# Kernel tuning notes

Hardware: AMD Instinct MI355X
Metric: run time of the kernel (lower is better)

Reference implementation:

```python
import jax, jax.numpy as jnp
import numpy as np
from jax import lax

# Dims from LSTMTagger class constants
B, S, LP = 1024, 128, 14       # sentences, words/sentence, padded chars/word
K, CE, WE, Lf = 3, 6, 10, 4    # char window, char emb, word emb, cnn filters
H, V, A, T = 6, 50000, 100, 135  # lstm hidden, vocab, alphabet, tagset
D = WE + Lf                     # lstm input dim = 14
LW = LP - K + 1                 # conv windows per word = 12


def setup_inputs() -> dict:
    key = jax.random.key(0)
    ks = jax.random.split(key, 14)
    n = lambda k, shp: jax.random.normal(k, shp, dtype=jnp.float32) * 0.1
    inp = {
        "word_idx": jax.random.randint(ks[0], (B, S), 0, V, dtype=jnp.int32),
        "char_idx": jax.random.randint(ks[1], (B, S, LP), 0, A, dtype=jnp.int32),
        "word_emb": n(ks[2], (V, WE)),
        "char_emb": n(ks[3], (A, CE)),
        "Wc": n(ks[4], (Lf, K * CE)),   # Conv1d(1, l, K*CE) weight, squeezed
        "bc": n(ks[5], (Lf,)),
        "Wih_f": n(ks[6], (4 * H, D)),
        "Whh_f": n(ks[7], (4 * H, H)),
        "b_f": n(ks[8], (4 * H,)),      # b_ih + b_hh fused (equivalent)
        "Wih_b": n(ks[9], (4 * H, D)),
        "Whh_b": n(ks[10], (4 * H, H)),
        "b_b": n(ks[11], (4 * H,)),
        "Wt": n(ks[12], (T, 2 * H)),
        "bt": n(ks[13], (T,)),
    }
    return inp


def _lstm_scan(xs, Wih, Whh, b):
    # xs: [S, B, D] -> hs: [S, B, H]; torch gate order i, f, g, o
    h0 = jnp.zeros((xs.shape[1], H), xs.dtype)

    def step(carry, xt):
        h, c = carry
        g = xt @ Wih.T + h @ Whh.T + b
        i, f, gg, o = jnp.split(g, 4, axis=-1)
        c = jax.nn.sigmoid(f) * c + jax.nn.sigmoid(i) * jnp.tanh(gg)
        h = jax.nn.sigmoid(o) * jnp.tanh(c)
        return (h, c), h

    _, hs = lax.scan(step, (h0, h0), xs)
    return hs


def reference(word_emb, char_emb, Wc, bc, Wih_f, Whh_f, b_f,
              Wih_b, Whh_b, b_b, Wt, bt, word_idx, char_idx):
    # per-word char CNN: sliding K-char windows, flatten, linear, max-pool
    ce = char_emb[char_idx]                              # [B,S,LP,CE]
    windows = jnp.concatenate([ce[:, :, i:i + LW] for i in range(K)], axis=-1)  # [B,S,LW,K*CE]
    phi = jnp.einsum('bswk,lk->bswl', windows, Wc) + bc  # [B,S,LW,Lf]
    char_repr = phi.max(axis=2)                          # [B,S,Lf]

    we = word_emb[word_idx]                              # [B,S,WE]
    x = jnp.concatenate([we, char_repr], axis=-1)        # [B,S,D]

    xs = x.transpose(1, 0, 2)                            # [S,B,D]
    hf = _lstm_scan(xs, Wih_f, Whh_f, b_f)               # forward direction
    hb = _lstm_scan(xs[::-1], Wih_b, Whh_b, b_b)[::-1]   # backward direction
    out = jnp.concatenate([hf, hb], axis=-1).transpose(1, 0, 2)  # [B,S,2H]

    tag_space = out @ Wt.T + bt                          # [B,S,T]
    return jax.nn.log_softmax(tag_space, axis=-1)
```

## Files before the change

### kernel.cpp

```cpp
#include <hip/hip_runtime.h>

#define B_   1024
#define S_   128
#define LP_  14
#define K_   3
#define CE_  6
#define WE_  10
#define LF_  4
#define H_   6
#define D_   14
#define T_   135
#define LW_  12
#define V_   50000
#define A_   100

static __device__ __forceinline__ float fsigm(float x) {
    return __frcp_rn(1.0f + __expf(-x));
}
static __device__ __forceinline__ float ftanh(float x) {
    return fmaf(2.0f, __frcp_rn(1.0f + __expf(-2.0f * x)), -1.0f);
}

__global__ __launch_bounds__(256) void k_el(
    const int* __restrict__ word_idx, const int* __restrict__ char_idx,
    const float* __restrict__ word_emb, const float* __restrict__ char_emb,
    const float* __restrict__ Wc, const float* __restrict__ bc,
    const float* __restrict__ Wih_f, const float* __restrict__ Whh_f, const float* __restrict__ b_f,
    const float* __restrict__ Wih_b, const float* __restrict__ Whh_b, const float* __restrict__ b_b,
    float* __restrict__ hbuf)
{
    __shared__ float s_g[4][S_][49];
    __shared__ float s_h[4][S_][12];
    __shared__ float s_ce[A_ * CE_];
    __shared__ float s_wc[LF_ * K_ * CE_];
    __shared__ float s_bc[LF_];

    int t = threadIdx.x;
    for (int e = t; e < A_ * CE_; e += 256) s_ce[e] = char_emb[e];
    if (t < LF_ * K_ * CE_) s_wc[t] = Wc[t];
    if (t < LF_) s_bc[t] = bc[t];
    __syncthreads();

    int Wbase = blockIdx.x * 512;
    #pragma unroll
    for (int rep = 0; rep < 2; ++rep) {
        int wl = t + rep * 256;
        int sent = wl >> 7;
        int step = wl & (S_ - 1);
        int w  = Wbase + wl;

        const int2* ci2 = (const int2*)(char_idx + (size_t)w * LP_);
        int idxs[LP_];
        #pragma unroll
        for (int p = 0; p < 7; ++p) {
            int2 v = ci2[p];
            idxs[2 * p] = v.x; idxs[2 * p + 1] = v.y;
        }
        float ce[LP_][CE_];
        #pragma unroll
        for (int p = 0; p < LP_; ++p) {
            int idx = idxs[p];
            idx = idx < 0 ? 0 : (idx >= A_ ? A_ - 1 : idx);
            #pragma unroll
            for (int c = 0; c < CE_; ++c) ce[p][c] = s_ce[idx * CE_ + c];
        }
        float x[D_];
        #pragma unroll
        for (int l = 0; l < LF_; ++l) {
            float acc[LW_];
            float bl = s_bc[l];
            #pragma unroll
            for (int q = 0; q < LW_; ++q) acc[q] = bl;
            #pragma unroll
            for (int kk = 0; kk < K_; ++kk) {
                #pragma unroll
                for (int c = 0; c < CE_; ++c) {
                    float wv_ = s_wc[l * (K_ * CE_) + kk * CE_ + c];
                    #pragma unroll
                    for (int q = 0; q < LW_; ++q) acc[q] = fmaf(ce[q + kk][c], wv_, acc[q]);
                }
            }
            float m = acc[0];
            #pragma unroll
            for (int q = 1; q < LW_; ++q) m = fmaxf(m, acc[q]);
            x[WE_ + l] = m;
        }
        int wi = word_idx[w];
        wi = wi < 0 ? 0 : (wi >= V_ ? V_ - 1 : wi);
        const float2* wep = (const float2*)(word_emb + (size_t)wi * WE_);
        #pragma unroll
        for (int c = 0; c < WE_ / 2; ++c) {
            float2 v = wep[c];
            x[2 * c] = v.x; x[2 * c + 1] = v.y;
        }

        #pragma unroll
        for (int r = 0; r < 4 * H_; ++r) {
            float a = b_f[r];
            #pragma unroll
            for (int k = 0; k < D_; ++k) a = fmaf(Wih_f[r * D_ + k], x[k], a);
            s_g[sent][step][r] = a;
        }
        #pragma unroll
        for (int r = 0; r < 4 * H_; ++r) {
            float a = b_b[r];
            #pragma unroll
            for (int k = 0; k < D_; ++k) a = fmaf(Wih_b[r * D_ + k], x[k], a);
            s_g[sent][step][24 + r] = a;
        }
    }
    __syncthreads();

    {
        int wv2  = t >> 6;
        int lane = t & 63;
        int dir  = lane >> 5;
        int l    = lane & 31;
        bool act = (l < H_);
        int u    = act ? l : (H_ - 1);

        const float* Whh = dir ? Whh_b : Whh_f;
        float whh[4][H_];
        #pragma unroll
        for (int j = 0; j < 4; ++j)
            #pragma unroll
            for (int k = 0; k < H_; ++k)
                whh[j][k] = Whh[(j * H_ + u) * H_ + k];

        const float* gp = &s_g[wv2][dir ? (S_ - 1) : 0][dir * 24 + u];
        int gstride = dir ? -49 : 49;

        float hv[H_];
        #pragma unroll
        for (int k = 0; k < H_; ++k) hv[k] = 0.f;
        float c = 0.f;

        float g0 = gp[0], g1 = gp[6], g2 = gp[12], g3 = gp[18];
        for (int s = 0; s < S_; ++s) {
            float ai = g0, af = g1, ag = g2, ao = g3;
            if (s + 1 < S_) {
                gp += gstride;
                g0 = gp[0]; g1 = gp[6]; g2 = gp[12]; g3 = gp[18];
            }
            #pragma unroll
            for (int k = 0; k < H_; ++k) {
                ai = fmaf(whh[0][k], hv[k], ai);
                af = fmaf(whh[1][k], hv[k], af);
                ag = fmaf(whh[2][k], hv[k], ag);
                ao = fmaf(whh[3][k], hv[k], ao);
            }
            float si = fsigm(ai);
            float sf = fsigm(af);
            float so = fsigm(ao);
            float tg = ftanh(ag);
            c = fmaf(sf, c, si * tg);
            float hu = so * ftanh(c);

            int se = dir ? (S_ - 1 - s) : s;
            if (act) s_h[wv2][se][dir * H_ + u] = hu;

            #pragma unroll
            for (int k = 0; k < H_; ++k) {
                int vf = __builtin_amdgcn_readlane(__float_as_int(hu), k);
                int vb = __builtin_amdgcn_readlane(__float_as_int(hu), 32 + k);
                hv[k] = __int_as_float(dir ? vb : vf);
            }
        }
    }
    __syncthreads();

    {
        float4* dst = (float4*)(hbuf + (size_t)blockIdx.x * 4 * S_ * 12);
        const float4* src = (const float4*)&s_h[0][0][0];
        #pragma unroll
        for (int i = 0; i < 6; ++i) dst[t + 256 * i] = src[t + 256 * i];
    }
}

__global__ __launch_bounds__(256) void k_p(
    const float* __restrict__ hbuf,
    const float* __restrict__ Wt, const float* __restrict__ bt,
    float* __restrict__ out)
{
    __shared__ float s_hb[64 * 12];
    int t = threadIdx.x;
    int ib = blockIdx.x * 64;
    {
        const float4* src = (const float4*)(hbuf + (size_t)ib * 12);
        float4* dst = (float4*)s_hb;
        if (t < 192) dst[t] = src[t];
    }
    __syncthreads();

    int lane = t & 63, wv = t >> 6;
    bool has2 = (lane < T_ - 128);
    int t2c = has2 ? (lane + 128) : (T_ - 1);

    float wA[12], wB[12], wC[12];
    #pragma unroll
    for (int jj = 0; jj < 12; ++jj) {
        wA[jj] = Wt[lane * 12 + jj];
        wB[jj] = Wt[(lane + 64) * 12 + jj];
        wC[jj] = Wt[t2c * 12 + jj];
    }
    float bA = bt[lane], bB = bt[lane + 64], bC = bt[t2c];

    int it0 = wv * 16;
    #pragma unroll 4
    for (int k = 0; k < 16; ++k) {
        int it = it0 + k;
        const float4* h4 = (const float4*)(s_hb + it * 12);
        float4 a0 = h4[0], a1 = h4[1], a2 = h4[2];
        float hv[12] = {a0.x, a0.y, a0.z, a0.w, a1.x, a1.y, a1.z, a1.w, a2.x, a2.y, a2.z, a2.w};
        float y0 = bA, y1 = bB, y2 = bC;
        #pragma unroll
        for (int jj = 0; jj < 12; ++jj) {
            y0 = fmaf(hv[jj], wA[jj], y0);
            y1 = fmaf(hv[jj], wB[jj], y1);
            y2 = fmaf(hv[jj], wC[jj], y2);
        }
        float ss = __expf(y0) + __expf(y1) + (has2 ? __expf(y2) : 0.0f);
        #pragma unroll
        for (int mk = 1; mk < 64; mk <<= 1) ss += __shfl_xor(ss, mk, 64);
        float ls = __logf(ss);
        float* op = out + (size_t)(ib + it) * T_;
        op[lane]      = y0 - ls;
        op[lane + 64] = y1 - ls;
        if (has2) op[lane + 128] = y2 - ls;
    }
}

extern "C" void kernel_launch(void* const* d_in, const int* in_sizes, int n_in,
                              void* d_out, int out_size, void* d_ws, size_t ws_size,
                              hipStream_t stream)
{
    const int* word_idx = (const int*)d_in[0];
    const int* char_idx = (const int*)d_in[1];
    const float* word_emb = (const float*)d_in[2];
    const float* char_emb = (const float*)d_in[3];
    const float* Wc    = (const float*)d_in[4];
    const float* bc    = (const float*)d_in[5];
    const float* Wih_f = (const float*)d_in[6];
    const float* Whh_f = (const float*)d_in[7];
    const float* b_f   = (const float*)d_in[8];
    const float* Wih_b = (const float*)d_in[9];
    const float* Whh_b = (const float*)d_in[10];
    const float* b_b   = (const float*)d_in[11];
    const float* Wt    = (const float*)d_in[12];
    const float* bt    = (const float*)d_in[13];

    float* hbuf = (float*)d_ws;

    k_el<<<B_ / 4, 256, 0, stream>>>(word_idx, char_idx, word_emb, char_emb, Wc, bc,
                                     Wih_f, Whh_f, b_f, Wih_b, Whh_b, b_b, hbuf);
    k_p<<<(B_ * S_) / 64, 256, 0, stream>>>(hbuf, Wt, bt, (float*)d_out);
}
```

Measured before the change: 186.9 us.

## Split fused embed+LSTM kernel into separate embed and recurrence kernels

Splits the fused embedding/CNN/input-projection plus recurrence kernel into two kernels. The first computes input gate pre-activations for all words and writes them to a global buffer laid out time-major. The second runs the recurrences with 8 sequences (both directions) per 64-thread wave, broadcasting h through shuffles and software-prefetching two steps ahead. This aims to raise occupancy and the number of concurrent recurrences, since the old kernel left most lanes idle and used large shared memory. In exchange it adds a global round trip for the gate buffer and reuses d_out as scratch when the workspace is too small.

```diff
diff --git a/kernel.cpp b/kernel.cpp
--- a/kernel.cpp
+++ b/kernel.cpp
@@ -13,6 +13,7 @@
 #define LW_  12
 #define V_   50000
 #define A_   100
+#define NSEQ (B_ * 2)
 
 static __device__ __forceinline__ float fsigm(float x) {
     return __frcp_rn(1.0f + __expf(-x));
@@ -21,160 +22,170 @@
     return fmaf(2.0f, __frcp_rn(1.0f + __expf(-2.0f * x)), -1.0f);
 }
 
-__global__ __launch_bounds__(256) void k_el(
+__global__ __launch_bounds__(256) void k_e(
     const int* __restrict__ word_idx, const int* __restrict__ char_idx,
     const float* __restrict__ word_emb, const float* __restrict__ char_emb,
     const float* __restrict__ Wc, const float* __restrict__ bc,
-    const float* __restrict__ Wih_f, const float* __restrict__ Whh_f, const float* __restrict__ b_f,
-    const float* __restrict__ Wih_b, const float* __restrict__ Whh_b, const float* __restrict__ b_b,
-    float* __restrict__ hbuf)
-{
-    __shared__ float s_g[4][S_][49];
-    __shared__ float s_h[4][S_][12];
+    const float* __restrict__ Wih_f, const float* __restrict__ b_f,
+    const float* __restrict__ Wih_b, const float* __restrict__ b_b,
+    float* __restrict__ gbuf)
+{
     __shared__ float s_ce[A_ * CE_];
     __shared__ float s_wc[LF_ * K_ * CE_];
     __shared__ float s_bc[LF_];
-
     int t = threadIdx.x;
     for (int e = t; e < A_ * CE_; e += 256) s_ce[e] = char_emb[e];
     if (t < LF_ * K_ * CE_) s_wc[t] = Wc[t];
     if (t < LF_) s_bc[t] = bc[t];
     __syncthreads();
 
-    int Wbase = blockIdx.x * 512;
-    #pragma unroll
-    for (int rep = 0; rep < 2; ++rep) {
-        int wl = t + rep * 256;
-        int sent = wl >> 7;
-        int step = wl & (S_ - 1);
-        int w  = Wbase + wl;
-
-        const int2* ci2 = (const int2*)(char_idx + (size_t)w * LP_);
-        int idxs[LP_];
-        #pragma unroll
-        for (int p = 0; p < 7; ++p) {
-            int2 v = ci2[p];
-            idxs[2 * p] = v.x; idxs[2 * p + 1] = v.y;
-        }
-        float ce[LP_][CE_];
-        #pragma unroll
-        for (int p = 0; p < LP_; ++p) {
-            int idx = idxs[p];
-            idx = idx < 0 ? 0 : (idx >= A_ ? A_ - 1 : idx);
+    int wid = blockIdx.x * 256 + t;
+    int s = wid >> 10;
+    int b = wid & 1023;
+    int w = b * S_ + s;
+
+    const int2* ci2 = (const int2*)(char_idx + (size_t)w * LP_);
+    int idxs[LP_];
+    #pragma unroll
+    for (int p = 0; p < 7; ++p) {
+        int2 v = ci2[p];
+        idxs[2 * p] = v.x; idxs[2 * p + 1] = v.y;
+    }
+    float ce[LP_][CE_];
+    #pragma unroll
+    for (int p = 0; p < LP_; ++p) {
+        int idx = idxs[p];
+        idx = idx < 0 ? 0 : (idx >= A_ ? A_ - 1 : idx);
+        #pragma unroll
+        for (int c = 0; c < CE_; ++c) ce[p][c] = s_ce[idx * CE_ + c];
+    }
+    float x[D_];
+    #pragma unroll
+    for (int l = 0; l < LF_; ++l) {
+        float acc[LW_];
+        float bl = s_bc[l];
+        #pragma unroll
+        for (int q = 0; q < LW_; ++q) acc[q] = bl;
+        #pragma unroll
+        for (int kk = 0; kk < K_; ++kk) {
             #pragma unroll
-            for (int c = 0; c < CE_; ++c) ce[p][c] = s_ce[idx * CE_ + c];
-        }
-        float x[D_];
-        #pragma unroll
-        for (int l = 0; l < LF_; ++l) {
-            float acc[LW_];
-            float bl = s_bc[l];
-            #pragma unroll
-            for (int q = 0; q < LW_; ++q) acc[q] = bl;
-            #pragma unroll
-            for (int kk = 0; kk < K_; ++kk) {
+            for (int c = 0; c < CE_; ++c) {
+                float wv_ = s_wc[l * (K_ * CE_) + kk * CE_ + c];
                 #pragma unroll
-                for (int c = 0; c < CE_; ++c) {
-                    float wv_ = s_wc[l * (K_ * CE_) + kk * CE_ + c];
-                    #pragma unroll
-                    for (int q = 0; q < LW_; ++q) acc[q] = fmaf(ce[q + kk][c], wv_, acc[q]);
-                }
+                for (int q = 0; q < LW_; ++q) acc[q] = fmaf(ce[q + kk][c], wv_, acc[q]);
             }
-            float m = acc[0];
-            #pragma unroll
-            for (int q = 1; q < LW_; ++q) m = fmaxf(m, acc[q]);
-            x[WE_ + l] = m;
-        }
-        int wi = word_idx[w];
-        wi = wi < 0 ? 0 : (wi >= V_ ? V_ - 1 : wi);
-        const float2* wep = (const float2*)(word_emb + (size_t)wi * WE_);
-        #pragma unroll
-        for (int c = 0; c < WE_ / 2; ++c) {
-            float2 v = wep[c];
-            x[2 * c] = v.x; x[2 * c + 1] = v.y;
-        }
-
-        #pragma unroll
-        for (int r = 0; r < 4 * H_; ++r) {
+        }
+        float m = acc[0];
+        #pragma unroll
+        for (int q = 1; q < LW_; ++q) m = fmaxf(m, acc[q]);
+        x[WE_ + l] = m;
+    }
+    int wi = word_idx[w];
+    wi = wi < 0 ? 0 : (wi >= V_ ? V_ - 1 : wi);
+    const float2* wep = (const float2*)(word_emb + (size_t)wi * WE_);
+    #pragma unroll
+    for (int c = 0; c < WE_ / 2; ++c) {
+        float2 v = wep[c];
+        x[2 * c] = v.x; x[2 * c + 1] = v.y;
+    }
+
+    float* dst = gbuf + ((size_t)s * NSEQ + 2 * b) * 24;
+    {
+        float g[24];
+        #pragma unroll
+        for (int r = 0; r < 24; ++r) {
             float a = b_f[r];
             #pragma unroll
             for (int k = 0; k < D_; ++k) a = fmaf(Wih_f[r * D_ + k], x[k], a);
-            s_g[sent][step][r] = a;
-        }
-        #pragma unroll
-        for (int r = 0; r < 4 * H_; ++r) {
+            g[r] = a;
+        }
+        #pragma unroll
+        for (int q = 0; q < 6; ++q)
+            ((float4*)dst)[q] = make_float4(g[4 * q], g[4 * q + 1], g[4 * q + 2], g[4 * q + 3]);
+    }
+    {
+        float g[24];
+        #pragma unroll
+        for (int r = 0; r < 24; ++r) {
             float a = b_b[r];
             #pragma unroll
             for (int k = 0; k < D_; ++k) a = fmaf(Wih_b[r * D_ + k], x[k], a);
-            s_g[sent][step][24 + r] = a;
-        }
-    }
-    __syncthreads();
-
-    {
-        int wv2  = t >> 6;
-        int lane = t & 63;
-        int dir  = lane >> 5;
-        int l    = lane & 31;
-        bool act = (l < H_);
-        int u    = act ? l : (H_ - 1);
-
-        const float* Whh = dir ? Whh_b : Whh_f;
-        float whh[4][H_];
-        #pragma unroll
-        for (int j = 0; j < 4; ++j)
-            #pragma unroll
-            for (int k = 0; k < H_; ++k)
-                whh[j][k] = Whh[(j * H_ + u) * H_ + k];
-
-        const float* gp = &s_g[wv2][dir ? (S_ - 1) : 0][dir * 24 + u];
-        int gstride = dir ? -49 : 49;
-
-        float hv[H_];
-        #pragma unroll
-        for (int k = 0; k < H_; ++k) hv[k] = 0.f;
-        float c = 0.f;
-
-        float g0 = gp[0], g1 = gp[6], g2 = gp[12], g3 = gp[18];
-        for (int s = 0; s < S_; ++s) {
-            float ai = g0, af = g1, ag = g2, ao = g3;
-            if (s + 1 < S_) {
-                gp += gstride;
-                g0 = gp[0]; g1 = gp[6]; g2 = gp[12]; g3 = gp[18];
-            }
-            #pragma unroll
-            for (int k = 0; k < H_; ++k) {
-                ai = fmaf(whh[0][k], hv[k], ai);
-                af = fmaf(whh[1][k], hv[k], af);
-                ag = fmaf(whh[2][k], hv[k], ag);
-                ao = fmaf(whh[3][k], hv[k], ao);
-            }
-            float si = fsigm(ai);
-            float sf = fsigm(af);
-            float so = fsigm(ao);
-            float tg = ftanh(ag);
-            c = fmaf(sf, c, si * tg);
-            float hu = so * ftanh(c);
-
-            int se = dir ? (S_ - 1 - s) : s;
-            if (act) s_h[wv2][se][dir * H_ + u] = hu;
-
-            #pragma unroll
-            for (int k = 0; k < H_; ++k) {
-                int vf = __builtin_amdgcn_readlane(__float_as_int(hu), k);
-                int vb = __builtin_amdgcn_readlane(__float_as_int(hu), 32 + k);
-                hv[k] = __int_as_float(dir ? vb : vf);
-            }
-        }
-    }
-    __syncthreads();
-
-    {
-        float4* dst = (float4*)(hbuf + (size_t)blockIdx.x * 4 * S_ * 12);
-        const float4* src = (const float4*)&s_h[0][0][0];
-        #pragma unroll
-        for (int i = 0; i < 6; ++i) dst[t + 256 * i] = src[t + 256 * i];
-    }
+            g[r] = a;
+        }
+        #pragma unroll
+        for (int q = 0; q < 6; ++q)
+            ((float4*)(dst + 24))[q] = make_float4(g[4 * q], g[4 * q + 1], g[4 * q + 2], g[4 * q + 3]);
+    }
+}
+
+__global__ __launch_bounds__(64) void k_l(
+    const float* __restrict__ Whh_f, const float* __restrict__ Whh_b,
+    const float* __restrict__ gbuf, float* __restrict__ hbuf)
+{
+    int lane = threadIdx.x;
+    int grp  = lane >> 3;
+    int u8   = lane & 7;
+    bool act = (u8 < H_);
+    int u    = act ? u8 : (H_ - 1);
+    int seq  = blockIdx.x * 8 + grp;
+    int b    = seq >> 1;
+    int dir  = seq & 1;
+
+    const float* Whh = dir ? Whh_b : Whh_f;
+    float w0[H_], w1[H_], w2[H_], w3[H_];
+    #pragma unroll
+    for (int k = 0; k < H_; ++k) {
+        w0[k] = Whh[(0 * H_ + u) * H_ + k];
+        w1[k] = Whh[(1 * H_ + u) * H_ + k];
+        w2[k] = Whh[(2 * H_ + u) * H_ + k];
+        w3[k] = Whh[(3 * H_ + u) * H_ + k];
+    }
+
+    const float* gp = gbuf + ((size_t)(dir ? S_ - 1 : 0) * NSEQ + (size_t)seq) * 24 + u;
+    long gstride = (dir ? -1L : 1L) * (long)(NSEQ * 24);
+
+#define LD4(dstv, p) { dstv[0] = (p)[0]; dstv[1] = (p)[6]; dstv[2] = (p)[12]; dstv[3] = (p)[18]; }
+
+    float a0[4], a1[4], p0[4] = {0,0,0,0}, p1[4] = {0,0,0,0};
+    LD4(a0, gp);
+    LD4(a1, gp + gstride);
+    const float* gpn = gp + 2 * gstride;
+
+    float h[H_];
+    #pragma unroll
+    for (int k = 0; k < H_; ++k) h[k] = 0.f;
+    float c = 0.f;
+    int gb = grp << 3;
+
+#define STEP(gv, sidx)                                                          \
+    {                                                                           \
+        float ai = gv[0], af = gv[1], ag = gv[2], ao = gv[3];                   \
+        _Pragma("unroll")                                                       \
+        for (int k = 0; k < H_; ++k) {                                          \
+            ai = fmaf(w0[k], h[k], ai);                                         \
+            af = fmaf(w1[k], h[k], af);                                         \
+            ag = fmaf(w2[k], h[k], ag);                                         \
+            ao = fmaf(w3[k], h[k], ao);                                         \
+        }                                                                       \
+        float si = fsigm(ai), sf = fsigm(af), so = fsigm(ao), tg = ftanh(ag);   \
+        c = fmaf(sf, c, si * tg);                                               \
+        float hu = so * ftanh(c);                                               \
+        int se = dir ? (S_ - 1 - (sidx)) : (sidx);                              \
+        if (act) hbuf[((size_t)b * S_ + se) * 12 + dir * H_ + u] = hu;          \
+        _Pragma("unroll")                                                       \
+        for (int k = 0; k < H_; ++k) h[k] = __shfl(hu, gb + k, 64);             \
+    }
+
+    for (int s = 0; s < S_; s += 2) {
+        if (s + 2 < S_) { LD4(p0, gpn); gpn += gstride; }
+        STEP(a0, s);
+        if (s + 3 < S_) { LD4(p1, gpn); gpn += gstride; }
+        STEP(a1, s + 1);
+        #pragma unroll
+        for (int q = 0; q < 4; ++q) { a0[q] = p0[q]; a1[q] = p1[q]; }
+    }
+#undef STEP
+#undef LD4
 }
 
 __global__ __launch_bounds__(256) void k_p(
@@ -249,9 +260,19 @@
     const float* Wt    = (const float*)d_in[12];
     const float* bt    = (const float*)d_in[13];
 
+    const size_t hbuf_fl = (size_t)B_ * S_ * 12;
+    const size_t gbuf_fl = (size_t)S_ * NSEQ * 24;
+
     float* hbuf = (float*)d_ws;
-
-    k_el<<<B_ / 4, 256, 0, stream>>>(word_idx, char_idx, word_emb, char_emb, Wc, bc,
-                                     Wih_f, Whh_f, b_f, Wih_b, Whh_b, b_b, hbuf);
+    float* gbuf;
+    if (ws_size >= (hbuf_fl + gbuf_fl) * sizeof(float)) {
+        gbuf = (float*)d_ws + hbuf_fl;
+    } else {
+        gbuf = (float*)d_out;
+    }
+
+    k_e<<<(B_ * S_) / 256, 256, 0, stream>>>(word_idx, char_idx, word_emb, char_emb,
+                                             Wc, bc, Wih_f, b_f, Wih_b, b_b, gbuf);
+    k_l<<<NSEQ / 8, 64, 0, stream>>>(Whh_f, Whh_b, gbuf, hbuf);
     k_p<<<(B_ * S_) / 64, 256, 0, stream>>>(hbuf, Wt, bt, (float*)d_out);
 }
```

Result: slower. 192.0 us (+2.8%).
